# Kernel tuning notes

Measured on AMD Instinct MI355X. Metric: run time of the kernel, lower is better.

Reference implementation:

```python
import jax, jax.numpy as jnp
import numpy as np

N = 50000      # nodes
E = 800000     # edges (before self loops)
RNA, SS, H, G = 645, 6, 128, 200
EPS = 1e-5

def setup_inputs() -> dict:
    key = jax.random.key(0)
    ks = jax.random.split(key, 16)
    def rn(k, shape, s=0.05):
        return jax.random.normal(k, shape, jnp.float32) * s
    return {
        "rna_embeddings": jax.random.normal(ks[0], (N, RNA), jnp.float32),
        "ss_emb": jax.random.normal(ks[1], (N, SS), jnp.float32),
        "edge_index": jax.random.randint(ks[2], (2, E), 0, N),
        "batch": jnp.sort(jax.random.randint(ks[3], (N,), 0, G)),
        "W_fuse": rn(ks[4], (RNA + SS, H)), "b_fuse": jnp.zeros((H,), jnp.float32),
        "ln1_g": jnp.ones((H,), jnp.float32), "ln1_b": jnp.zeros((H,), jnp.float32),
        "W_gat": rn(ks[5], (H, H)), "att_src": rn(ks[6], (H,)), "att_dst": rn(ks[7], (H,)),
        "b_gat": jnp.zeros((H,), jnp.float32),
        "gn_w": jnp.ones((H,), jnp.float32), "gn_b": jnp.zeros((H,), jnp.float32), "gn_ms": jnp.ones((H,), jnp.float32),
        "W_gate": rn(ks[8], (2 * H, H)), "b_gate": jnp.zeros((H,), jnp.float32),
        "W_head": rn(ks[9], (H, H)), "b_head": jnp.zeros((H,), jnp.float32),
        "ln2_g": jnp.ones((H,), jnp.float32), "ln2_b": jnp.zeros((H,), jnp.float32),
        "W_fc1": rn(ks[10], (H, H // 2)), "b_fc1": jnp.zeros((H // 2,), jnp.float32),
        "ln3_g": jnp.ones((H // 2,), jnp.float32), "ln3_b": jnp.zeros((H // 2,), jnp.float32),
        "W_fc2": rn(ks[11], (H // 2, 1)), "b_fc2": jnp.zeros((1,), jnp.float32),
    }

def _ln(x, g, b):
    m = jnp.mean(x, -1, keepdims=True)
    v = jnp.mean(jnp.square(x - m), -1, keepdims=True)
    return (x - m) * jax.lax.rsqrt(v + EPS) * g + b

def _graphnorm(x, batch, w, b, ms):
    cnt = jax.ops.segment_sum(jnp.ones((x.shape[0], 1), x.dtype), batch, num_segments=G)
    mean = jax.ops.segment_sum(x, batch, num_segments=G) / jnp.maximum(cnt, 1.0)
    out = x - ms * mean[batch]
    var = jax.ops.segment_sum(jnp.square(out), batch, num_segments=G) / jnp.maximum(cnt, 1.0)
    std = jnp.sqrt(var + EPS)
    return w * out / std[batch] + b

def _gat(x, src, dst, W, a_src, a_dst, bias):
    xw = x @ W                                     # [N,H]
    e = (xw @ a_src)[src] + (xw @ a_dst)[dst]      # per-edge score
    e = jax.nn.leaky_relu(e, 0.2)
    m = jax.ops.segment_max(e, dst, num_segments=N)  # every dst has a self loop
    e = jnp.exp(e - m[dst])
    s = jax.ops.segment_sum(e, dst, num_segments=N)
    alpha = e / (s[dst] + 1e-16)
    return jax.ops.segment_sum(alpha[:, None] * xw[src], dst, num_segments=N) + bias

def reference(rna_embeddings, ss_emb, edge_index, batch,
              W_fuse, b_fuse, ln1_g, ln1_b,
              W_gat, att_src, att_dst, b_gat,
              gn_w, gn_b, gn_ms,
              W_gate, b_gate, W_head, b_head, ln2_g, ln2_b,
              W_fc1, b_fc1, ln3_g, ln3_b, W_fc2, b_fc2):
    loop = jnp.arange(N)
    src = jnp.concatenate([edge_index[0], loop])   # PyG GATConv add_self_loops=True
    dst = jnp.concatenate([edge_index[1], loop])
    h = jax.nn.relu(_ln(jnp.concatenate([rna_embeddings, ss_emb], -1) @ W_fuse + b_fuse, ln1_g, ln1_b))
    h_res = h
    h = jax.nn.relu(_graphnorm(_gat(h, src, dst, W_gat, att_src, att_dst, b_gat), batch, gn_w, gn_b, gn_ms))
    h1 = h
    h = jax.nn.relu(_graphnorm(_gat(h1, src, dst, W_gat, att_src, att_dst, b_gat), batch, gn_w, gn_b, gn_ms))
    h2 = h + h_res
    gate = jax.nn.sigmoid(jnp.concatenate([h1, h2], -1) @ W_gate + b_gate)
    h = gate * h1 + (1.0 - gate) * h2
    h = jax.nn.relu(_ln(h @ W_head + b_head, ln2_g, ln2_b))
    h = jax.nn.relu(_ln(h @ W_fc1 + b_fc1, ln3_g, ln3_b))
    return (h @ W_fc2 + b_fc2)[:, 0]
```

## Files before the change

### kernel.cpp

```cpp
#include <hip/hip_runtime.h>
#include <hip/hip_bf16.h>
#include <math.h>

#define NN 50000
#define EE 800000
#define RNA_D 645
#define KFUSE 651
#define KPACK 704
#define HD 128
#define GG 200
#define SAK 72
#define HGS 136

typedef __attribute__((ext_vector_type(8))) short shortx8;
typedef __attribute__((ext_vector_type(4))) float floatx4;

__device__ __forceinline__ float lrelu(float x){ return x >= 0.f ? x : 0.2f*x; }
__device__ __forceinline__ short f2bf(float x){
  union { __hip_bfloat16 h; short s; } u; u.h = __float2bfloat16(x); return u.s;
}
__device__ __forceinline__ float bf2f(short s){
  union { float f; unsigned u; } c; c.u = ((unsigned)(unsigned short)s) << 16; return c.f;
}
__device__ __forceinline__ float2 upk(unsigned u){
  union { float f; unsigned v; } a, b;
  a.v = u << 16; b.v = u & 0xffff0000u;
  return make_float2(a.f, b.f);
}

__launch_bounds__(256)
__global__ void pack_kernel(const float* __restrict__ rna, const float* __restrict__ ss,
                            short* __restrict__ Abf){
  int row = blockIdx.x*2 + (threadIdx.x >> 7);
  int t = threadIdx.x & 127;
  if (row >= NN) return;
  const float* rrow = rna + (size_t)row*RNA_D;
  short* orow = Abf + (size_t)row*KPACK;
  #pragma unroll
  for (int j=0;j<6;++j){
    int c = t + j*128;
    if (c < KPACK){
      float v = 0.f;
      if (c < RNA_D) v = rrow[c];
      else if (c < KFUSE) v = ss[row*6 + (c - RNA_D)];
      orow[c] = f2bf(v);
    }
  }
}

__global__ void hist_gstart_kernel(const int* __restrict__ dst, int* __restrict__ deg,
                                   const int* __restrict__ batch, int* __restrict__ gstart){
  int e = blockIdx.x*256 + threadIdx.x;
  if (e < EE) atomicAdd(&deg[dst[e]], 1);
  if (e < NN){
    int g = batch[e];
    if (e == 0){ for (int gg=0; gg<=g; ++gg) gstart[gg] = 0; }
    else { int gp = batch[e-1]; for (int gg=gp+1; gg<=g; ++gg) gstart[gg] = e; }
    if (e == NN-1){ for (int gg=g+1; gg<=GG; ++gg) gstart[gg] = NN; }
  }
}
__global__ void scan1_kernel(const int* __restrict__ deg, int* __restrict__ row_start,
                             int* __restrict__ blocksum){
  __shared__ int s[256];
  int i = blockIdx.x*256 + threadIdx.x;
  int v = (i < NN) ? deg[i] : 0;
  s[threadIdx.x] = v;
  __syncthreads();
  for (int off=1; off<256; off<<=1){
    int t = (threadIdx.x >= off) ? s[threadIdx.x-off] : 0;
    __syncthreads();
    s[threadIdx.x] += t;
    __syncthreads();
  }
  if (i < NN) row_start[i] = s[threadIdx.x] - v;
  if (threadIdx.x == 255) blocksum[blockIdx.x] = s[255];
}
__global__ void scan2_kernel(int* __restrict__ blocksum, int nb){
  __shared__ int s[256];
  int v = (threadIdx.x < nb) ? blocksum[threadIdx.x] : 0;
  s[threadIdx.x] = v;
  __syncthreads();
  for (int off=1; off<256; off<<=1){
    int t = (threadIdx.x >= off) ? s[threadIdx.x-off] : 0;
    __syncthreads();
    s[threadIdx.x] += t;
    __syncthreads();
  }
  blocksum[threadIdx.x] = s[threadIdx.x] - v;
}
__global__ void scan3_kernel(int* __restrict__ row_start, const int* __restrict__ blocksum,
                             int* __restrict__ cursor){
  int i = blockIdx.x*256 + threadIdx.x;
  if (i < NN){
    int v = row_start[i] + blocksum[blockIdx.x];
    row_start[i] = v;
    cursor[i] = v;
  }
  if (i == 0) row_start[NN] = EE;
}
__global__ void scatter_kernel(const int* __restrict__ srcl, const int* __restrict__ dstl,
                               int* __restrict__ cursor, int* __restrict__ csr_src){
  int e = blockIdx.x*256 + threadIdx.x;
  if (e >= EE) return;
  int d = dstl[e];
  int slot = atomicAdd(&cursor[d], 1);
  csr_src[slot] = srcl[e];
}

__global__ void wprep_all_kernel(const float* __restrict__ Wf, const float* __restrict__ Wg,
                                 const float* __restrict__ Wgt, const float* __restrict__ Wh,
                                 const float* __restrict__ W1,
                                 short* __restrict__ Tf, short* __restrict__ Tg,
                                 short* __restrict__ Tgt, short* __restrict__ Th,
                                 short* __restrict__ T1){
  int idx = blockIdx.x*256 + threadIdx.x;
  const int S0=128*KPACK, S1=128*128, S2=128*256, S3=128*128, S4=64*128;
  if (idx < S0){ int n=idx/KPACK, k=idx-n*KPACK; Tf[idx]=f2bf(k<KFUSE ? Wf[k*128+n] : 0.f); return; }
  idx -= S0;
  if (idx < S1){ int n=idx>>7, k=idx&127; Tg[idx]=f2bf(Wg[k*128+n]); return; }
  idx -= S1;
  if (idx < S2){ int n=idx>>8, k=idx&255; Tgt[idx]=f2bf(Wgt[k*128+n]); return; }
  idx -= S2;
  if (idx < S3){ int n=idx>>7, k=idx&127; Th[idx]=f2bf(Wh[k*128+n]); return; }
  idx -= S3;
  if (idx < S4){ int n=idx>>7, k=idx&127; T1[idx]=f2bf(W1[k*64+n]); return; }
}

template<int MODE, int NT, bool GNA>
__launch_bounds__(256)
__global__ void mfma_gemm(const float* __restrict__ A0,
                          const short* __restrict__ Apk,
                          const short* __restrict__ Wt, const float* __restrict__ bias,
                          const float* __restrict__ gw, const float* __restrict__ gb,
                          const float* __restrict__ as_, const float* __restrict__ ad_,
                          const int* __restrict__ batch, const float* __restrict__ gnsh,
                          const float* __restrict__ gnsc, float* __restrict__ side,
                          float* __restrict__ out, short* __restrict__ outb,
                          float* __restrict__ es, float* __restrict__ ed,
                          int K, int Kp){
  __shared__ short sA[128*SAK];
  __shared__ short sB[NT*16*SAK];
  const int tid  = threadIdx.x;
  const int wave = tid >> 6, lane = tid & 63;
  const int quad = lane >> 4, l16 = lane & 15;
  const int rowBase = blockIdx.x * 128;
  const int NCOL = NT*16;

  floatx4 acc[2][NT];
  #pragma unroll
  for (int t=0;t<2;++t)
    #pragma unroll
    for (int ct=0;ct<NT;++ct)
      #pragma unroll
      for (int j=0;j<4;++j) acc[t][ct][j] = 0.f;

  const int srow = tid >> 1, shalf = tid & 1;
  const int sgr = rowBase + srow;

  for (int k0 = 0; k0 < K; k0 += 64){
    if (MODE == 0){
      #pragma unroll
      for (int j=0;j<4;++j){
        int flat = tid + j*256;
        int r = flat >> 3, c8 = flat & 7;
        int gr = rowBase + r;
        shortx8 v = {0,0,0,0,0,0,0,0};
        if (gr < NN) v = *(const shortx8*)&Apk[(size_t)gr*KPACK + k0 + c8*8];
        *(shortx8*)&sA[r*SAK + c8*8] = v;
      }
    } else {
      int kb = k0 + shalf*32;
      short tmp[32];
      if (GNA){
        int g = (sgr < NN) ? batch[sgr] : 0;
        const float* py  = A0 + (size_t)sgr*HD + kb;
        const float* psh = gnsh + g*HD + kb;
        const float* psc = gnsc + g*HD + kb;
        const float* pbb = gb + kb;
        #pragma unroll
        for (int q4=0;q4<8;++q4){
          float4 yv = (sgr < NN) ? *(const float4*)(py + q4*4) : make_float4(0.f,0.f,0.f,0.f);
          float4 sh = *(const float4*)(psh + q4*4);
          float4 sc = *(const float4*)(psc + q4*4);
          float4 bb = *(const float4*)(pbb + q4*4);
          float4 v;
          v.x = fmaxf((yv.x - sh.x)*sc.x + bb.x, 0.f);
          v.y = fmaxf((yv.y - sh.y)*sc.y + bb.y, 0.f);
          v.z = fmaxf((yv.z - sh.z)*sc.z + bb.z, 0.f);
          v.w = fmaxf((yv.w - sh.w)*sc.w + bb.w, 0.f);
          if (sgr < NN) *(float4*)&side[(size_t)sgr*HD + kb + q4*4] = v;
          tmp[q4*4+0]=f2bf(v.x); tmp[q4*4+1]=f2bf(v.y);
          tmp[q4*4+2]=f2bf(v.z); tmp[q4*4+3]=f2bf(v.w);
        }
      } else {
        const float* p = A0 + (size_t)sgr*HD + kb;
        #pragma unroll
        for (int q4=0;q4<8;++q4){
          float4 f = (sgr < NN) ? *(const float4*)(p + q4*4) : make_float4(0.f,0.f,0.f,0.f);
          tmp[q4*4+0]=f2bf(f.x); tmp[q4*4+1]=f2bf(f.y);
          tmp[q4*4+2]=f2bf(f.z); tmp[q4*4+3]=f2bf(f.w);
        }
      }
      #pragma unroll
      for (int q8=0;q8<4;++q8)
        *(shortx8*)&sA[srow*SAK + shalf*32 + q8*8] = *(shortx8*)&tmp[q8*8];
    }
    {
      int col = tid >> 1, kb = k0 + (tid&1)*32;
      #pragma unroll
      for (int q8=0;q8<4;++q8)
        *(shortx8*)&sB[col*SAK + (tid&1)*32 + q8*8] = *(const shortx8*)&Wt[(size_t)col*Kp + kb + q8*8];
    }
    __syncthreads();
    #pragma unroll
    for (int ks=0; ks<2; ++ks){
      int kb = ks*32 + quad*8;
      shortx8 af0 = *(const shortx8*)&sA[(wave*32 +      l16)*SAK + kb];
      shortx8 af1 = *(const shortx8*)&sA[(wave*32 + 16 + l16)*SAK + kb];
      #pragma unroll
      for (int ct=0; ct<NT; ++ct){
        shortx8 bf = *(const shortx8*)&sB[(ct*16 + l16)*SAK + kb];
        acc[0][ct] = __builtin_amdgcn_mfma_f32_16x16x32_bf16(af0, bf, acc[0][ct], 0,0,0);
        acc[1][ct] = __builtin_amdgcn_mfma_f32_16x16x32_bf16(af1, bf, acc[1][ct], 0,0,0);
      }
    }
    __syncthreads();
  }

  if (MODE == 1){
    float asv[NT], adv[NT];
    #pragma unroll
    for (int ct=0;ct<NT;++ct){ asv[ct] = as_[ct*16+l16]; adv[ct] = ad_[ct*16+l16]; }
    #pragma unroll
    for (int t=0;t<2;++t)
      #pragma unroll
      for (int i=0;i<4;++i){
        int gr = rowBase + wave*32 + t*16 + quad*4 + i;
        float s=0.f, d=0.f;
        #pragma unroll
        for (int ct=0;ct<NT;++ct){
          float v = acc[t][ct][i];
          s = fmaf(v, asv[ct], s); d = fmaf(v, adv[ct], d);
          if (gr < NN) outb[(size_t)gr*HD + ct*16 + l16] = f2bf(v);
        }
        #pragma unroll
        for (int off=1; off<16; off<<=1){ s += __shfl_xor(s,off); d += __shfl_xor(d,off); }
        if (l16 == 0 && gr < NN){ es[gr] = s; ed[gr] = d; }
      }
  } else {
    float biasv[NT], gv[NT], bv[NT];
    #pragma unroll
    for (int ct=0;ct<NT;++ct){
      biasv[ct] = bias[ct*16+l16]; gv[ct] = gw[ct*16+l16]; bv[ct] = gb[ct*16+l16];
    }
    #pragma unroll
    for (int t=0;t<2;++t)
      #pragma unroll
      for (int i=0;i<4;++i){
        int gr = rowBase + wave*32 + t*16 + quad*4 + i;
        float v[NT]; float s=0.f, q=0.f;
        #pragma unroll
        for (int ct=0;ct<NT;++ct){
          v[ct] = acc[t][ct][i] + biasv[ct];
          s += v[ct]; q = fmaf(v[ct], v[ct], q);
        }
        #pragma unroll
        for (int off=1; off<16; off<<=1){ s += __shfl_xor(s,off); q += __shfl_xor(q,off); }
        float mean = s * (1.f/NCOL);
        float inv  = rsqrtf(q*(1.f/NCOL) - mean*mean + 1e-5f);
        if (gr < NN){
          #pragma unroll
          for (int ct=0;ct<NT;++ct)
            out[(size_t)gr*NCOL + ct*16 + l16] = fmaxf((v[ct]-mean)*inv*gv[ct] + bv[ct], 0.f);
        }
      }
  }
}

__launch_bounds__(256)
__global__ void gat_aggregate_kernel(const short* __restrict__ xwb, const float* __restrict__ es,
                                     const float* __restrict__ ed, const int* __restrict__ row_start,
                                     const int* __restrict__ csr_src, const float* __restrict__ bgat,
                                     float* __restrict__ out){
  int gid = blockIdx.x*256 + threadIdx.x;
  int n = gid >> 6, lane = gid & 63;
  if (n >= NN) return;
  int beg = row_start[n], end = row_start[n+1];
  float edn = ed[n];
  float sc_self = lrelu(es[n] + edn);

  int i0 = beg + lane;
  bool v0 = i0 < end;
  int sA = v0 ? csr_src[i0] : 0;
  float eA = v0 ? lrelu(es[sA] + edn) : -3.0e38f;
  float m = fmaxf(sc_self, eA);
  for (int i = beg + 64 + lane; i < end; i += 64)
    m = fmaxf(m, lrelu(es[csr_src[i]] + edn));
  #pragma unroll
  for (int off=1; off<64; off<<=1) m = fmaxf(m, __shfl_xor(m, off));

  float wA = v0 ? __expf(eA - m) : 0.f;
  float wsum_l = wA;
  float wself = __expf(sc_self - m);
  float2 self2 = upk(*(const unsigned*)&xwb[(size_t)n*HD + 2*lane]);
  float a0 = wself*self2.x, a1 = wself*self2.y;

  int deg0 = min(end - beg, 64);
  int j = 0;
  for (; j + 8 <= deg0; j += 8){
    int ss[8]; float ww[8]; unsigned xv[8];
    #pragma unroll
    for (int u=0;u<8;++u){ ss[u]=__shfl(sA,j+u); ww[u]=__shfl(wA,j+u); }
    #pragma unroll
    for (int u=0;u<8;++u) xv[u] = *(const unsigned*)&xwb[(size_t)ss[u]*HD + 2*lane];
    #pragma unroll
    for (int u=0;u<8;++u){ float2 f=upk(xv[u]); a0=fmaf(ww[u],f.x,a0); a1=fmaf(ww[u],f.y,a1); }
  }
  for (; j < deg0; ++j){
    int s=__shfl(sA,j); float w=__shfl(wA,j);
    float2 f = upk(*(const unsigned*)&xwb[(size_t)s*HD + 2*lane]);
    a0=fmaf(w,f.x,a0); a1=fmaf(w,f.y,a1);
  }
  for (int c = beg + 64; c < end; c += 64){
    int i = c + lane;
    bool vb = i < end;
    int sB = vb ? csr_src[i] : 0;
    float wB = vb ? __expf(lrelu(es[sB] + edn) - m) : 0.f;
    wsum_l += wB;
    int degc = min(end - c, 64);
    for (int jj=0; jj<degc; ++jj){
      int s=__shfl(sB,jj); float w=__shfl(wB,jj);
      float2 f = upk(*(const unsigned*)&xwb[(size_t)s*HD + 2*lane]);
      a0=fmaf(w,f.x,a0); a1=fmaf(w,f.y,a1);
    }
  }
  #pragma unroll
  for (int off=1; off<64; off<<=1) wsum_l += __shfl_xor(wsum_l, off);
  float dinv = 1.f/(wsum_l + wself + 1e-16f);
  float2 b2 = *(const float2*)&bgat[2*lane];
  float2 o; o.x = a0*dinv + b2.x; o.y = a1*dinv + b2.y;
  *(float2*)&out[(size_t)n*HD + 2*lane] = o;
}

__launch_bounds__(256)
__global__ void gn_group_kernel(const float* __restrict__ x, const int* __restrict__ gstart,
                                const float* __restrict__ gnw, const float* __restrict__ gnms,
                                float* __restrict__ shiftv, float* __restrict__ scalev){
  int g = blockIdx.x;
  int n0 = gstart[g], n1 = gstart[g+1];
  int f = threadIdx.x & 127, half = threadIdx.x >> 7;
  float s = 0.f, q = 0.f;
  for (int n = n0 + half; n < n1; n += 2){
    float v = x[(size_t)n*HD + f];
    s += v; q = fmaf(v, v, q);
  }
  __shared__ float rs[256], rq[256];
  rs[threadIdx.x] = s; rq[threadIdx.x] = q;
  __syncthreads();
  if (threadIdx.x < 128){
    s = rs[threadIdx.x] + rs[threadIdx.x+128];
    q = rq[threadIdx.x] + rq[threadIdx.x+128];
    float c = fmaxf((float)(n1 - n0), 1.f);
    float mean = s / c;
    float ms = gnms[f];
    float var = q/c - mean*mean*ms*(2.f - ms);
    shiftv[g*HD+f] = ms*mean;
    scalev[g*HD+f] = gnw[f] / sqrtf(var + 1e-5f);
  }
}

__launch_bounds__(256)
__global__ void tail_kernel(const float* __restrict__ h1, const float* __restrict__ y2,
                            const float* __restrict__ hres, const int* __restrict__ batch,
                            const float* __restrict__ gnsh, const float* __restrict__ gnsc,
                            const float* __restrict__ gnb,
                            const short* __restrict__ Wt_gate, const float* __restrict__ b_gate,
                            const short* __restrict__ Wt_head, const float* __restrict__ b_head,
                            const float* __restrict__ ln2g, const float* __restrict__ ln2b,
                            const short* __restrict__ Wt_fc1, const float* __restrict__ b_fc1,
                            const float* __restrict__ ln3g, const float* __restrict__ ln3b,
                            const float* __restrict__ W_fc2, const float* __restrict__ b_fc2,
                            float* __restrict__ outp){
  __shared__ short hgL[128*HGS];
  __shared__ short sA[128*SAK];
  __shared__ short sB[128*SAK];
  const int tid = threadIdx.x, wave = tid>>6, lane = tid&63;
  const int quad = lane>>4, l16 = lane&15;
  const int rowBase = blockIdx.x*128;
  const int srow = tid>>1, shalf = tid&1;
  const int sgr = rowBase + srow;

  floatx4 acc[2][8];
  #pragma unroll
  for (int t=0;t<2;++t)
    #pragma unroll
    for (int ct=0;ct<8;++ct)
      #pragma unroll
      for (int j=0;j<4;++j) acc[t][ct][j]=0.f;

  for (int c2=0; c2<4; ++c2){
    int kb = c2*64 + shalf*32;
    short tmp[32];
    if (kb < 128){
      const float* p = h1 + (size_t)sgr*HD + kb;
      #pragma unroll
      for (int q4=0;q4<8;++q4){
        float4 f = (sgr < NN) ? *(const float4*)(p + q4*4) : make_float4(0.f,0.f,0.f,0.f);
        tmp[q4*4+0]=f2bf(f.x); tmp[q4*4+1]=f2bf(f.y);
        tmp[q4*4+2]=f2bf(f.z); tmp[q4*4+3]=f2bf(f.w);
      }
    } else {
      int cb = kb - 128;
      int g = (sgr < NN) ? batch[sgr] : 0;
      const float* py  = y2   + (size_t)sgr*HD + cb;
      const float* ph  = hres + (size_t)sgr*HD + cb;
      const float* psh = gnsh + g*HD + cb;
      const float* psc = gnsc + g*HD + cb;
      const float* pbb = gnb + cb;
      #pragma unroll
      for (int q4=0;q4<8;++q4){
        float4 yv = (sgr < NN) ? *(const float4*)(py + q4*4) : make_float4(0.f,0.f,0.f,0.f);
        float4 hv = (sgr < NN) ? *(const float4*)(ph + q4*4) : make_float4(0.f,0.f,0.f,0.f);
        float4 sh = *(const float4*)(psh + q4*4);
        float4 sc = *(const float4*)(psc + q4*4);
        float4 bb = *(const float4*)(pbb + q4*4);
        float4 v;
        v.x = fmaxf((yv.x - sh.x)*sc.x + bb.x, 0.f) + hv.x;
        v.y = fmaxf((yv.y - sh.y)*sc.y + bb.y, 0.f) + hv.y;
        v.z = fmaxf((yv.z - sh.z)*sc.z + bb.z, 0.f) + hv.z;
        v.w = fmaxf((yv.w - sh.w)*sc.w + bb.w, 0.f) + hv.w;
        tmp[q4*4+0]=f2bf(v.x); tmp[q4*4+1]=f2bf(v.y);
        tmp[q4*4+2]=f2bf(v.z); tmp[q4*4+3]=f2bf(v.w);
      }
      #pragma unroll
      for (int q8=0;q8<4;++q8)
        *(shortx8*)&hgL[srow*HGS + cb + q8*8] = *(shortx8*)&tmp[q8*8];
    }
    #pragma unroll
    for (int q8=0;q8<4;++q8)
      *(shortx8*)&sA[srow*SAK + shalf*32 + q8*8] = *(shortx8*)&tmp[q8*8];
    {
      int col = tid >> 1, kb2 = c2*64 + (tid&1)*32;
      #pragma unroll
      for (int q8=0;q8<4;++q8)
        *(shortx8*)&sB[col*SAK + (tid&1)*32 + q8*8] = *(const shortx8*)&Wt_gate[(size_t)col*256 + kb2 + q8*8];
    }
    __syncthreads();
    #pragma unroll
    for (int ks=0; ks<2; ++ks){
      int kk = ks*32 + quad*8;
      shortx8 af0 = *(const shortx8*)&sA[(wave*32 +      l16)*SAK + kk];
      shortx8 af1 = *(const shortx8*)&sA[(wave*32 + 16 + l16)*SAK + kk];
      #pragma unroll
      for (int ct=0; ct<8; ++ct){
        shortx8 bf = *(const shortx8*)&sB[(ct*16 + l16)*SAK + kk];
        acc[0][ct] = __builtin_amdgcn_mfma_f32_16x16x32_bf16(af0, bf, acc[0][ct], 0,0,0);
        acc[1][ct] = __builtin_amdgcn_mfma_f32_16x16x32_bf16(af1, bf, acc[1][ct], 0,0,0);
      }
    }
    __syncthreads();
  }
  {
    float biasv[8];
    #pragma unroll
    for (int ct=0;ct<8;++ct) biasv[ct] = b_gate[ct*16+l16];
    #pragma unroll
    for (int t=0;t<2;++t)
      #pragma unroll
      for (int i=0;i<4;++i){
        int row = wave*32 + t*16 + quad*4 + i;
        int gr = rowBase + row;
        #pragma unroll
        for (int ct=0;ct<8;++ct){
          int c = ct*16 + l16;
          float g = 1.f/(1.f + __expf(-(acc[t][ct][i] + biasv[ct])));
          float x1 = (gr < NN) ? h1[(size_t)gr*HD + c] : 0.f;
          float x2 = bf2f(hgL[row*HGS + c]);
          hgL[row*HGS + c] = f2bf(g*x1 + (1.f-g)*x2);
        }
      }
  }
  __syncthreads();

  floatx4 acc2[2][8];
  #pragma unroll
  for (int t=0;t<2;++t)
    #pragma unroll
    for (int ct=0;ct<8;++ct)
      #pragma unroll
      for (int j=0;j<4;++j) acc2[t][ct][j]=0.f;
  for (int c2=0;c2<2;++c2){
    {
      int col = tid >> 1, kb2 = c2*64 + (tid&1)*32;
      #pragma unroll
      for (int q8=0;q8<4;++q8)
        *(shortx8*)&sB[col*SAK + (tid&1)*32 + q8*8] = *(const shortx8*)&Wt_head[(size_t)col*128 + kb2 + q8*8];
    }
    __syncthreads();
    #pragma unroll
    for (int ks=0; ks<2; ++ks){
      int kg = c2*64 + ks*32 + quad*8;
      int kk = ks*32 + quad*8;
      shortx8 af0 = *(const shortx8*)&hgL[(wave*32 +      l16)*HGS + kg];
      shortx8 af1 = *(const shortx8*)&hgL[(wave*32 + 16 + l16)*HGS + kg];
      #pragma unroll
      for (int ct=0; ct<8; ++ct){
        shortx8 bf = *(const shortx8*)&sB[(ct*16 + l16)*SAK + kk];
        acc2[0][ct] = __builtin_amdgcn_mfma_f32_16x16x32_bf16(af0, bf, acc2[0][ct], 0,0,0);
        acc2[1][ct] = __builtin_amdgcn_mfma_f32_16x16x32_bf16(af1, bf, acc2[1][ct], 0,0,0);
      }
    }
    __syncthreads();
  }
  {
    float biasv[8], gv[8], bv[8];
    #pragma unroll
    for (int ct=0;ct<8;++ct){
      biasv[ct] = b_head[ct*16+l16]; gv[ct] = ln2g[ct*16+l16]; bv[ct] = ln2b[ct*16+l16];
    }
    #pragma unroll
    for (int t=0;t<2;++t)
      #pragma unroll
      for (int i=0;i<4;++i){
        int row = wave*32 + t*16 + quad*4 + i;
        float v[8]; float s=0.f, q=0.f;
        #pragma unroll
        for (int ct=0;ct<8;++ct){
          v[ct] = acc2[t][ct][i] + biasv[ct];
          s += v[ct]; q = fmaf(v[ct], v[ct], q);
        }
        #pragma unroll
        for (int off=1; off<16; off<<=1){ s += __shfl_xor(s,off); q += __shfl_xor(q,off); }
        float mean = s * (1.f/128.f);
        float inv  = rsqrtf(q*(1.f/128.f) - mean*mean + 1e-5f);
        #pragma unroll
        for (int ct=0;ct<8;++ct)
          hgL[row*HGS + ct*16 + l16] = f2bf(fmaxf((v[ct]-mean)*inv*gv[ct] + bv[ct], 0.f));
      }
  }
  __syncthreads();

  floatx4 acc3[2][4];
  #pragma unroll
  for (int t=0;t<2;++t)
    #pragma unroll
    for (int ct=0;ct<4;++ct)
      #pragma unroll
      for (int j=0;j<4;++j) acc3[t][ct][j]=0.f;
  for (int c2=0;c2<2;++c2){
    if (tid < 128){
      int col = tid >> 1, kb2 = c2*64 + (tid&1)*32;
      #pragma unroll
      for (int q8=0;q8<4;++q8)
        *(shortx8*)&sB[col*SAK + (tid&1)*32 + q8*8] = *(const shortx8*)&Wt_fc1[(size_t)col*128 + kb2 + q8*8];
    }
    __syncthreads();
    #pragma unroll
    for (int ks=0; ks<2; ++ks){
      int kg = c2*64 + ks*32 + quad*8;
      int kk = ks*32 + quad*8;
      shortx8 af0 = *(const shortx8*)&hgL[(wave*32 +      l16)*HGS + kg];
      shortx8 af1 = *(const shortx8*)&hgL[(wave*32 + 16 + l16)*HGS + kg];
      #pragma unroll
      for (int ct=0; ct<4; ++ct){
        shortx8 bf = *(const shortx8*)&sB[(ct*16 + l16)*SAK + kk];
        acc3[0][ct] = __builtin_amdgcn_mfma_f32_16x16x32_bf16(af0, bf, acc3[0][ct], 0,0,0);
        acc3[1][ct] = __builtin_amdgcn_mfma_f32_16x16x32_bf16(af1, bf, acc3[1][ct], 0,0,0);
      }
    }
    __syncthreads();
  }
  {
    float biasv[4], gv[4], bv[4], w2v[4];
    #pragma unroll
    for (int ct=0;ct<4;++ct){
      biasv[ct] = b_fc1[ct*16+l16]; gv[ct] = ln3g[ct*16+l16]; bv[ct] = ln3b[ct*16+l16];
      w2v[ct] = W_fc2[ct*16+l16];
    }
    float b2 = b_fc2[0];
    #pragma unroll
    for (int t=0;t<2;++t)
      #pragma unroll
      for (int i=0;i<4;++i){
        int gr = rowBase + wave*32 + t*16 + quad*4 + i;
        float v[4]; float s=0.f, q=0.f;
        #pragma unroll
        for (int ct=0;ct<4;++ct){
          v[ct] = acc3[t][ct][i] + biasv[ct];
          s += v[ct]; q = fmaf(v[ct], v[ct], q);
        }
        #pragma unroll
        for (int off=1; off<16; off<<=1){ s += __shfl_xor(s,off); q += __shfl_xor(q,off); }
        float mean = s * (1.f/64.f);
        float inv  = rsqrtf(q*(1.f/64.f) - mean*mean + 1e-5f);
        float p = 0.f;
        #pragma unroll
        for (int ct=0;ct<4;++ct){
          float o = fmaxf((v[ct]-mean)*inv*gv[ct] + bv[ct], 0.f);
          p = fmaf(o, w2v[ct], p);
        }
        #pragma unroll
        for (int off=1; off<16; off<<=1) p += __shfl_xor(p, off);
        if (l16 == 0 && gr < NN) outp[gr] = p + b2;
      }
  }
}

extern "C" void kernel_launch(void* const* d_in, const int* in_sizes, int n_in,
                              void* d_out, int out_size, void* d_ws, size_t ws_size,
                              hipStream_t stream){
  const float* rna    = (const float*)d_in[0];
  const float* ss     = (const float*)d_in[1];
  const int*   eidx   = (const int*)d_in[2];
  const int*   batch  = (const int*)d_in[3];
  const float* W_fuse = (const float*)d_in[4];
  const float* b_fuse = (const float*)d_in[5];
  const float* ln1_g  = (const float*)d_in[6];
  const float* ln1_b  = (const float*)d_in[7];
  const float* W_gat  = (const float*)d_in[8];
  const float* att_src= (const float*)d_in[9];
  const float* att_dst= (const float*)d_in[10];
  const float* b_gat  = (const float*)d_in[11];
  const float* gn_w   = (const float*)d_in[12];
  const float* gn_b   = (const float*)d_in[13];
  const float* gn_ms  = (const float*)d_in[14];
  const float* W_gate = (const float*)d_in[15];
  const float* b_gate = (const float*)d_in[16];
  const float* W_head = (const float*)d_in[17];
  const float* b_head = (const float*)d_in[18];
  const float* ln2_g  = (const float*)d_in[19];
  const float* ln2_b  = (const float*)d_in[20];
  const float* W_fc1  = (const float*)d_in[21];
  const float* b_fc1  = (const float*)d_in[22];
  const float* ln3_g  = (const float*)d_in[23];
  const float* ln3_b  = (const float*)d_in[24];
  const float* W_fc2  = (const float*)d_in[25];
  const float* b_fc2  = (const float*)d_in[26];
  float* outp = (float*)d_out;

  const int* srcl = eidx;
  const int* dstl = eidx + EE;

  char* base = (char*)d_ws;
  size_t off = 0;
  auto alloc = [&](size_t bytes)->void*{
    void* p = base + off; off = (off + bytes + 255) & ~(size_t)255; return p;
  };
  float* h    = (float*)alloc((size_t)NN*HD*4);
  float* h1   = (float*)alloc((size_t)NN*HD*4);
  float* y    = (float*)alloc((size_t)NN*HD*4);
  short* xwb  = (short*)alloc((size_t)NN*HD*2);
  float* es   = (float*)alloc((size_t)NN*4);
  float* ed   = (float*)alloc((size_t)NN*4);
  float* shiftv = (float*)alloc(GG*HD*4);
  float* scalev = (float*)alloc(GG*HD*4);
  int* deg       = (int*)alloc((size_t)NN*4);
  int* row_start = (int*)alloc((size_t)(NN+1)*4);
  int* cursor    = (int*)alloc((size_t)NN*4);
  int* csr_src   = (int*)alloc((size_t)EE*4);
  int* blocksum  = (int*)alloc(256*4);
  int* gstart    = (int*)alloc((GG+1)*4);
  short* Abf     = (short*)alloc((size_t)NN*KPACK*2);
  short* Wt_fuse = (short*)alloc((size_t)128*KPACK*2);
  short* Wt_gat  = (short*)alloc((size_t)128*128*2);
  short* Wt_gate = (short*)alloc((size_t)128*256*2);
  short* Wt_head = (short*)alloc((size_t)128*128*2);
  short* Wt_fc1  = (short*)alloc((size_t)64*128*2);

  const int NB  = (NN + 255)/256;
  const int GB  = (NN + 127)/128;
  const int EB  = (EE + 255)/256;
  const int WVB = (NN*64 + 255)/256;
  const int WPREP_TOT = 128*KPACK + 128*128 + 128*256 + 128*128 + 64*128;

  pack_kernel<<<(NN+1)/2, 256, 0, stream>>>(rna, ss, Abf);
  wprep_all_kernel<<<(WPREP_TOT+255)/256, 256, 0, stream>>>(
      W_fuse, W_gat, W_gate, W_head, W_fc1,
      Wt_fuse, Wt_gat, Wt_gate, Wt_head, Wt_fc1);

  hipMemsetAsync(deg, 0, (size_t)NN*4, stream);
  hist_gstart_kernel<<<EB, 256, 0, stream>>>(dstl, deg, batch, gstart);
  scan1_kernel<<<NB, 256, 0, stream>>>(deg, row_start, blocksum);
  scan2_kernel<<<1, 256, 0, stream>>>(blocksum, NB);
  scan3_kernel<<<NB, 256, 0, stream>>>(row_start, blocksum, cursor);
  scatter_kernel<<<EB, 256, 0, stream>>>(srcl, dstl, cursor, csr_src);

  mfma_gemm<0,8,false><<<GB, 256, 0, stream>>>(nullptr, Abf, Wt_fuse, b_fuse, ln1_g, ln1_b,
      nullptr, nullptr, nullptr, nullptr, nullptr, nullptr, h, nullptr, nullptr, nullptr, KPACK, KPACK);

  mfma_gemm<1,8,false><<<GB, 256, 0, stream>>>(h, nullptr, Wt_gat, nullptr, nullptr, nullptr,
      att_src, att_dst, nullptr, nullptr, nullptr, nullptr, nullptr, xwb, es, ed, HD, HD);
  gat_aggregate_kernel<<<WVB, 256, 0, stream>>>(xwb, es, ed, row_start, csr_src, b_gat, y);
  gn_group_kernel<<<GG, 256, 0, stream>>>(y, gstart, gn_w, gn_ms, shiftv, scalev);

  mfma_gemm<1,8,true><<<GB, 256, 0, stream>>>(y, nullptr, Wt_gat, nullptr, nullptr, gn_b,
      att_src, att_dst, batch, shiftv, scalev, h1, nullptr, xwb, es, ed, HD, HD);
  gat_aggregate_kernel<<<WVB, 256, 0, stream>>>(xwb, es, ed, row_start, csr_src, b_gat, y);
  gn_group_kernel<<<GG, 256, 0, stream>>>(y, gstart, gn_w, gn_ms, shiftv, scalev);

  tail_kernel<<<GB, 256, 0, stream>>>(h1, y, h, batch, shiftv, scalev, gn_b,
      Wt_gate, b_gate, Wt_head, b_head, ln2_g, ln2_b,
      Wt_fc1, b_fc1, ln3_g, ln3_b, W_fc2, b_fc2, outp);
}
```

Baseline: 628.8 us.

## Fuse input packing, fuse GEMM+LayerNorm, and first GAT projection into one kernel

Removes the separate bf16 pack pass over the 50000x704 input. The fuse GEMM now reads fp32 rna/ss rows directly and converts them while staging into shared memory. The LayerNorm output is kept in shared memory as bf16 and fed straight into the W_gat projection in the same kernel, which eliminates a re-read of h and one launch. GraphNorm statistics now use 1024-thread blocks to raise parallelism per group. The costs are higher LDS usage, which may cut occupancy, and unvectorized scalar fp32 loads from rna rows, which have an odd stride.

```diff
diff --git a/kernel.cpp b/kernel.cpp
--- a/kernel.cpp
+++ b/kernel.cpp
@@ -26,26 +26,6 @@
   union { float f; unsigned v; } a, b;
   a.v = u << 16; b.v = u & 0xffff0000u;
   return make_float2(a.f, b.f);
-}
-
-__launch_bounds__(256)
-__global__ void pack_kernel(const float* __restrict__ rna, const float* __restrict__ ss,
-                            short* __restrict__ Abf){
-  int row = blockIdx.x*2 + (threadIdx.x >> 7);
-  int t = threadIdx.x & 127;
-  if (row >= NN) return;
-  const float* rrow = rna + (size_t)row*RNA_D;
-  short* orow = Abf + (size_t)row*KPACK;
-  #pragma unroll
-  for (int j=0;j<6;++j){
-    int c = t + j*128;
-    if (c < KPACK){
-      float v = 0.f;
-      if (c < RNA_D) v = rrow[c];
-      else if (c < KFUSE) v = ss[row*6 + (c - RNA_D)];
-      orow[c] = f2bf(v);
-    }
-  }
 }
 
 __global__ void hist_gstart_kernel(const int* __restrict__ dst, int* __restrict__ deg,
@@ -124,6 +104,166 @@
   if (idx < S3){ int n=idx>>7, k=idx&127; Th[idx]=f2bf(Wh[k*128+n]); return; }
   idx -= S3;
   if (idx < S4){ int n=idx>>7, k=idx&127; T1[idx]=f2bf(W1[k*64+n]); return; }
+}
+
+__launch_bounds__(256)
+__global__ void fuse_xw_kernel(const float* __restrict__ rna, const float* __restrict__ ss,
+                               const short* __restrict__ Wtf, const float* __restrict__ bfu,
+                               const float* __restrict__ g1, const float* __restrict__ b1,
+                               const short* __restrict__ Wtg,
+                               const float* __restrict__ as_, const float* __restrict__ ad_,
+                               float* __restrict__ hout, short* __restrict__ xwb,
+                               float* __restrict__ es, float* __restrict__ ed){
+  __shared__ short sA[128*SAK];
+  __shared__ short sB[128*SAK];
+  __shared__ short hA[128*HGS];
+  const int tid  = threadIdx.x;
+  const int wave = tid >> 6, lane = tid & 63;
+  const int quad = lane >> 4, l16 = lane & 15;
+  const int rowBase = blockIdx.x * 128;
+  const int srow = tid >> 1, shalf = tid & 1;
+  const int sgr = rowBase + srow;
+
+  floatx4 acc[2][8];
+  #pragma unroll
+  for (int t=0;t<2;++t)
+    #pragma unroll
+    for (int ct=0;ct<8;++ct)
+      #pragma unroll
+      for (int j=0;j<4;++j) acc[t][ct][j] = 0.f;
+
+  for (int k0 = 0; k0 < KPACK; k0 += 64){
+    {
+      short tmp[32];
+      if (sgr < NN && k0 < 640){
+        const float* rrow = rna + (size_t)sgr*RNA_D + k0 + shalf*32;
+        #pragma unroll
+        for (int j=0;j<32;++j) tmp[j] = f2bf(rrow[j]);
+      } else if (sgr < NN){
+        int cb = k0 + shalf*32;
+        #pragma unroll
+        for (int j=0;j<32;++j){
+          int c = cb + j;
+          float v = 0.f;
+          if (c < RNA_D) v = rna[(size_t)sgr*RNA_D + c];
+          else if (c < KFUSE) v = ss[sgr*6 + (c - RNA_D)];
+          tmp[j] = f2bf(v);
+        }
+      } else {
+        #pragma unroll
+        for (int j=0;j<32;++j) tmp[j] = 0;
+      }
+      #pragma unroll
+      for (int q8=0;q8<4;++q8)
+        *(shortx8*)&sA[srow*SAK + shalf*32 + q8*8] = *(shortx8*)&tmp[q8*8];
+    }
+    {
+      int col = tid >> 1, kb = k0 + (tid&1)*32;
+      #pragma unroll
+      for (int q8=0;q8<4;++q8)
+        *(shortx8*)&sB[col*SAK + (tid&1)*32 + q8*8] = *(const shortx8*)&Wtf[(size_t)col*KPACK + kb + q8*8];
+    }
+    __syncthreads();
+    #pragma unroll
+    for (int ks=0; ks<2; ++ks){
+      int kb = ks*32 + quad*8;
+      shortx8 af0 = *(const shortx8*)&sA[(wave*32 +      l16)*SAK + kb];
+      shortx8 af1 = *(const shortx8*)&sA[(wave*32 + 16 + l16)*SAK + kb];
+      #pragma unroll
+      for (int ct=0; ct<8; ++ct){
+        shortx8 bf = *(const shortx8*)&sB[(ct*16 + l16)*SAK + kb];
+        acc[0][ct] = __builtin_amdgcn_mfma_f32_16x16x32_bf16(af0, bf, acc[0][ct], 0,0,0);
+        acc[1][ct] = __builtin_amdgcn_mfma_f32_16x16x32_bf16(af1, bf, acc[1][ct], 0,0,0);
+      }
+    }
+    __syncthreads();
+  }
+
+  {
+    float biasv[8], gv[8], bv[8];
+    #pragma unroll
+    for (int ct=0;ct<8;++ct){
+      biasv[ct] = bfu[ct*16+l16]; gv[ct] = g1[ct*16+l16]; bv[ct] = b1[ct*16+l16];
+    }
+    #pragma unroll
+    for (int t=0;t<2;++t)
+      #pragma unroll
+      for (int i=0;i<4;++i){
+        int row = wave*32 + t*16 + quad*4 + i;
+        int gr = rowBase + row;
+        float v[8]; float s=0.f, q=0.f;
+        #pragma unroll
+        for (int ct=0;ct<8;++ct){
+          v[ct] = acc[t][ct][i] + biasv[ct];
+          s += v[ct]; q = fmaf(v[ct], v[ct], q);
+        }
+        #pragma unroll
+        for (int off=1; off<16; off<<=1){ s += __shfl_xor(s,off); q += __shfl_xor(q,off); }
+        float mean = s * (1.f/128.f);
+        float inv  = rsqrtf(q*(1.f/128.f) - mean*mean + 1e-5f);
+        #pragma unroll
+        for (int ct=0;ct<8;++ct){
+          float o = fmaxf((v[ct]-mean)*inv*gv[ct] + bv[ct], 0.f);
+          if (gr < NN) hout[(size_t)gr*HD + ct*16 + l16] = o;
+          hA[row*HGS + ct*16 + l16] = f2bf(o);
+        }
+      }
+  }
+  __syncthreads();
+
+  floatx4 acc2[2][8];
+  #pragma unroll
+  for (int t=0;t<2;++t)
+    #pragma unroll
+    for (int ct=0;ct<8;++ct)
+      #pragma unroll
+      for (int j=0;j<4;++j) acc2[t][ct][j] = 0.f;
+
+  for (int c2=0; c2<2; ++c2){
+    {
+      int col = tid >> 1, kb2 = c2*64 + (tid&1)*32;
+      #pragma unroll
+      for (int q8=0;q8<4;++q8)
+        *(shortx8*)&sB[col*SAK + (tid&1)*32 + q8*8] = *(const shortx8*)&Wtg[(size_t)col*HD + kb2 + q8*8];
+    }
+    __syncthreads();
+    #pragma unroll
+    for (int ks=0; ks<2; ++ks){
+      int kg = c2*64 + ks*32 + quad*8;
+      int kk = ks*32 + quad*8;
+      shortx8 af0 = *(const shortx8*)&hA[(wave*32 +      l16)*HGS + kg];
+      shortx8 af1 = *(const shortx8*)&hA[(wave*32 + 16 + l16)*HGS + kg];
+      #pragma unroll
+      for (int ct=0; ct<8; ++ct){
+        shortx8 bf = *(const shortx8*)&sB[(ct*16 + l16)*SAK + kk];
+        acc2[0][ct] = __builtin_amdgcn_mfma_f32_16x16x32_bf16(af0, bf, acc2[0][ct], 0,0,0);
+        acc2[1][ct] = __builtin_amdgcn_mfma_f32_16x16x32_bf16(af1, bf, acc2[1][ct], 0,0,0);
+      }
+    }
+    __syncthreads();
+  }
+
+  {
+    float asv[8], adv[8];
+    #pragma unroll
+    for (int ct=0;ct<8;++ct){ asv[ct] = as_[ct*16+l16]; adv[ct] = ad_[ct*16+l16]; }
+    #pragma unroll
+    for (int t=0;t<2;++t)
+      #pragma unroll
+      for (int i=0;i<4;++i){
+        int gr = rowBase + wave*32 + t*16 + quad*4 + i;
+        float s=0.f, d=0.f;
+        #pragma unroll
+        for (int ct=0;ct<8;++ct){
+          float v = acc2[t][ct][i];
+          s = fmaf(v, asv[ct], s); d = fmaf(v, adv[ct], d);
+          if (gr < NN) xwb[(size_t)gr*HD + ct*16 + l16] = f2bf(v);
+        }
+        #pragma unroll
+        for (int off=1; off<16; off<<=1){ s += __shfl_xor(s,off); d += __shfl_xor(d,off); }
+        if (l16 == 0 && gr < NN){ es[gr] = s; ed[gr] = d; }
+      }
+  }
 }
 
 template<int MODE, int NT, bool GNA>
@@ -158,17 +298,7 @@
   const int sgr = rowBase + srow;
 
   for (int k0 = 0; k0 < K; k0 += 64){
-    if (MODE == 0){
-      #pragma unroll
-      for (int j=0;j<4;++j){
-        int flat = tid + j*256;
-        int r = flat >> 3, c8 = flat & 7;
-        int gr = rowBase + r;
-        shortx8 v = {0,0,0,0,0,0,0,0};
-        if (gr < NN) v = *(const shortx8*)&Apk[(size_t)gr*KPACK + k0 + c8*8];
-        *(shortx8*)&sA[r*SAK + c8*8] = v;
-      }
-    } else {
+    {
       int kb = k0 + shalf*32;
       short tmp[32];
       if (GNA){
@@ -227,7 +357,7 @@
     __syncthreads();
   }
 
-  if (MODE == 1){
+  {
     float asv[NT], adv[NT];
     #pragma unroll
     for (int ct=0;ct<NT;++ct){ asv[ct] = as_[ct*16+l16]; adv[ct] = ad_[ct*16+l16]; }
@@ -246,33 +376,6 @@
         #pragma unroll
         for (int off=1; off<16; off<<=1){ s += __shfl_xor(s,off); d += __shfl_xor(d,off); }
         if (l16 == 0 && gr < NN){ es[gr] = s; ed[gr] = d; }
-      }
-  } else {
-    float biasv[NT], gv[NT], bv[NT];
-    #pragma unroll
-    for (int ct=0;ct<NT;++ct){
-      biasv[ct] = bias[ct*16+l16]; gv[ct] = gw[ct*16+l16]; bv[ct] = gb[ct*16+l16];
-    }
-    #pragma unroll
-    for (int t=0;t<2;++t)
-      #pragma unroll
-      for (int i=0;i<4;++i){
-        int gr = rowBase + wave*32 + t*16 + quad*4 + i;
-        float v[NT]; float s=0.f, q=0.f;
-        #pragma unroll
-        for (int ct=0;ct<NT;++ct){
-          v[ct] = acc[t][ct][i] + biasv[ct];
-          s += v[ct]; q = fmaf(v[ct], v[ct], q);
-        }
-        #pragma unroll
-        for (int off=1; off<16; off<<=1){ s += __shfl_xor(s,off); q += __shfl_xor(q,off); }
-        float mean = s * (1.f/NCOL);
-        float inv  = rsqrtf(q*(1.f/NCOL) - mean*mean + 1e-5f);
-        if (gr < NN){
-          #pragma unroll
-          for (int ct=0;ct<NT;++ct)
-            out[(size_t)gr*NCOL + ct*16 + l16] = fmaxf((v[ct]-mean)*inv*gv[ct] + bv[ct], 0.f);
-        }
       }
   }
 }
@@ -342,20 +445,24 @@
   *(float2*)&out[(size_t)n*HD + 2*lane] = o;
 }
 
-__launch_bounds__(256)
+__launch_bounds__(1024)
 __global__ void gn_group_kernel(const float* __restrict__ x, const int* __restrict__ gstart,
                                 const float* __restrict__ gnw, const float* __restrict__ gnms,
                                 float* __restrict__ shiftv, float* __restrict__ scalev){
   int g = blockIdx.x;
   int n0 = gstart[g], n1 = gstart[g+1];
-  int f = threadIdx.x & 127, half = threadIdx.x >> 7;
+  int f = threadIdx.x & 127, slot = threadIdx.x >> 7;
   float s = 0.f, q = 0.f;
-  for (int n = n0 + half; n < n1; n += 2){
+  for (int n = n0 + slot; n < n1; n += 8){
     float v = x[(size_t)n*HD + f];
     s += v; q = fmaf(v, v, q);
   }
-  __shared__ float rs[256], rq[256];
+  __shared__ float rs[1024], rq[1024];
   rs[threadIdx.x] = s; rq[threadIdx.x] = q;
+  __syncthreads();
+  if (threadIdx.x < 512){ rs[threadIdx.x] += rs[threadIdx.x+512]; rq[threadIdx.x] += rq[threadIdx.x+512]; }
+  __syncthreads();
+  if (threadIdx.x < 256){ rs[threadIdx.x] += rs[threadIdx.x+256]; rq[threadIdx.x] += rq[threadIdx.x+256]; }
   __syncthreads();
   if (threadIdx.x < 128){
     s = rs[threadIdx.x] + rs[threadIdx.x+128];
@@ -660,7 +767,6 @@
   int* csr_src   = (int*)alloc((size_t)EE*4);
   int* blocksum  = (int*)alloc(256*4);
   int* gstart    = (int*)alloc((GG+1)*4);
-  short* Abf     = (short*)alloc((size_t)NN*KPACK*2);
   short* Wt_fuse = (short*)alloc((size_t)128*KPACK*2);
   short* Wt_gat  = (short*)alloc((size_t)128*128*2);
   short* Wt_gate = (short*)alloc((size_t)128*256*2);
@@ -673,7 +779,6 @@
   const int WVB = (NN*64 + 255)/256;
   const int WPREP_TOT = 128*KPACK + 128*128 + 128*256 + 128*128 + 64*128;
 
-  pack_kernel<<<(NN+1)/2, 256, 0, stream>>>(rna, ss, Abf);
   wprep_all_kernel<<<(WPREP_TOT+255)/256, 256, 0, stream>>>(
       W_fuse, W_gat, W_gate, W_head, W_fc1,
       Wt_fuse, Wt_gat, Wt_gate, Wt_head, Wt_fc1);
@@ -685,18 +790,16 @@
   scan3_kernel<<<NB, 256, 0, stream>>>(row_start, blocksum, cursor);
   scatter_kernel<<<EB, 256, 0, stream>>>(srcl, dstl, cursor, csr_src);
 
-  mfma_gemm<0,8,false><<<GB, 256, 0, stream>>>(nullptr, Abf, Wt_fuse, b_fuse, ln1_g, ln1_b,
-      nullptr, nullptr, nullptr, nullptr, nullptr, nullptr, h, nullptr, nullptr, nullptr, KPACK, KPACK);
-
-  mfma_gemm<1,8,false><<<GB, 256, 0, stream>>>(h, nullptr, Wt_gat, nullptr, nullptr, nullptr,
-      att_src, att_dst, nullptr, nullptr, nullptr, nullptr, nullptr, xwb, es, ed, HD, HD);
+  fuse_xw_kernel<<<GB, 256, 0, stream>>>(rna, ss, Wt_fuse, b_fuse, ln1_g, ln1_b,
+      Wt_gat, att_src, att_dst, h, xwb, es, ed);
+
   gat_aggregate_kernel<<<WVB, 256, 0, stream>>>(xwb, es, ed, row_start, csr_src, b_gat, y);
-  gn_group_kernel<<<GG, 256, 0, stream>>>(y, gstart, gn_w, gn_ms, shiftv, scalev);
+  gn_group_kernel<<<GG, 1024, 0, stream>>>(y, gstart, gn_w, gn_ms, shiftv, scalev);
 
   mfma_gemm<1,8,true><<<GB, 256, 0, stream>>>(y, nullptr, Wt_gat, nullptr, nullptr, gn_b,
       att_src, att_dst, batch, shiftv, scalev, h1, nullptr, xwb, es, ed, HD, HD);
   gat_aggregate_kernel<<<WVB, 256, 0, stream>>>(xwb, es, ed, row_start, csr_src, b_gat, y);
-  gn_group_kernel<<<GG, 256, 0, stream>>>(y, gstart, gn_w, gn_ms, shiftv, scalev);
+  gn_group_kernel<<<GG, 1024, 0, stream>>>(y, gstart, gn_w, gn_ms, shiftv, scalev);
 
   tail_kernel<<<GB, 256, 0, stream>>>(h1, y, h, batch, shiftv, scalev, gn_b,
       Wt_gate, b_gate, Wt_head, b_head, ln2_g, ln2_b,
```

New measurement: 558.6 us. 1.13x faster.
